# Performance work log

Hardware: AMD Instinct MI355X
Metric: run time of the kernel (lower is better)

The kernel has to match this reference:

```python
import jax, jax.numpy as jnp
import numpy as np

C = 256
B, H, W = 4, 64, 64


def _conv1x1(x, w, b):
    # 1x1 Conv2d == per-pixel channel matmul: w is [C_out, C_in]
    return jnp.einsum('oc,bchw->bohw', w, x) + b[None, :, None, None]


def setup_inputs() -> dict:
    key = jax.random.key(0)
    ks = jax.random.split(key, 9)
    s = 1.0 / np.sqrt(C)  # conv init scale
    return {
        'x': jax.random.normal(ks[0], (B, C, H, W), dtype=jnp.float32),
        'wq': jax.random.normal(ks[1], (C, C), dtype=jnp.float32) * s,
        'bq': jax.random.normal(ks[2], (C,), dtype=jnp.float32) * s,
        'wk': jax.random.normal(ks[3], (C, C), dtype=jnp.float32) * s,
        'bk': jax.random.normal(ks[4], (C,), dtype=jnp.float32) * s,
        'wv': jax.random.normal(ks[5], (C, C), dtype=jnp.float32) * s,
        'bv': jax.random.normal(ks[6], (C,), dtype=jnp.float32) * s,
        'wp': jax.random.normal(ks[7], (C, C), dtype=jnp.float32) * s,
        'bp': jax.random.normal(ks[8], (C,), dtype=jnp.float32) * s,
    }


def reference(x, wq, bq, wk, bk, wv, bv, wp, bp):
    b, c, h, w = x.shape
    n = h * w
    q = _conv1x1(x, wq, bq).reshape(b, c, n)
    k = _conv1x1(x, wk, bk).reshape(b, c, n)
    v = _conv1x1(x, wv, bv).reshape(b, c, n)
    attn = jnp.einsum('bci,bcj->bij', q, k) * (c ** -0.5)  # [B, N, N]
    # NOTE: original torch code softmaxes over dim=1 (the i axis), not -1
    attn = jax.nn.softmax(attn, axis=1)
    out = jnp.einsum('bij,bcj->bci', attn, v).reshape(b, c, h, w)
    return _conv1x1(out, wp, bp)
```

## Files before the change

### kernel.cpp

```cpp
#include <hip/hip_runtime.h>
#include <stdint.h>


#define DI __device__ __forceinline__
typedef __attribute__((ext_vector_type(4))) float f32x4;
typedef __attribute__((ext_vector_type(8))) short s16x8;
typedef __attribute__((ext_vector_type(4))) short s16x4;
typedef __attribute__((ext_vector_type(4))) unsigned short u16x4;

constexpr int C = 256;
constexpr int N = 4096;

DI unsigned short f2bf(float f) {
  unsigned int u = __float_as_uint(f);
  u += 0x7FFFu + ((u >> 16) & 1u);
  return (unsigned short)(u >> 16);
}
DI float bf2f(unsigned short s) { return __uint_as_float(((unsigned int)s) << 16); }

DI f32x4 mfma16(s16x8 a, s16x8 b, f32x4 c) {
  return __builtin_amdgcn_mfma_f32_16x16x32_bf16(a, b, c, 0, 0, 0);
}

__global__ __launch_bounds__(256) void kw_conv(
    const float* __restrict__ wq, const float* __restrict__ wk,
    const float* __restrict__ wv, const float* __restrict__ wp,
    unsigned short* __restrict__ WQ, unsigned short* __restrict__ WK,
    unsigned short* __restrict__ WV, unsigned short* __restrict__ WPH,
    unsigned short* __restrict__ WPL) {
  int idx = (blockIdx.x * 256 + threadIdx.x) * 4;
  f32x4 q = *(const f32x4*)(wq + idx);
  f32x4 k = *(const f32x4*)(wk + idx);
  f32x4 v = *(const f32x4*)(wv + idx);
  f32x4 p = *(const f32x4*)(wp + idx);
  u16x4 oq, ok, ov, oh, ol;
#pragma unroll
  for (int e = 0; e < 4; ++e) {
    oq[e] = f2bf(q[e] * 0.0625f);
    ok[e] = f2bf(k[e]);
    ov[e] = f2bf(v[e]);
    unsigned short h = f2bf(p[e]);
    oh[e] = h;
    ol[e] = f2bf(p[e] - bf2f(h));
  }
  *(u16x4*)(WQ + idx) = oq;
  *(u16x4*)(WK + idx) = ok;
  *(u16x4*)(WV + idx) = ov;
  *(u16x4*)(WPH + idx) = oh;
  *(u16x4*)(WPL + idx) = ol;
}

__global__ __launch_bounds__(256) void k0_transpose(const float* __restrict__ X,
                                                    unsigned short* __restrict__ XT) {
  __shared__ float tile[64 * 65];
  int t = threadIdx.x;
  int wg = blockIdx.x;
  int b = wg >> 8, rem = wg & 255;
  int c0 = (rem >> 6) * 64, n0 = (rem & 63) * 64;
  const float* xb = X + (size_t)b * C * N;
  int cl = t >> 2, ng = (t & 3) * 16;
#pragma unroll
  for (int k = 0; k < 4; ++k) {
    f32x4 v = *(const f32x4*)(xb + (size_t)(c0 + cl) * N + n0 + ng + k * 4);
#pragma unroll
    for (int e = 0; e < 4; ++e) tile[cl * 65 + ng + k * 4 + e] = v[e];
  }
  __syncthreads();
  int nl = t >> 2, cg = (t & 3) * 16;
  unsigned short* xtb = XT + (size_t)b * N * C;
  s16x8 o0v, o1v;
#pragma unroll
  for (int j = 0; j < 8; ++j) o0v[j] = (short)f2bf(tile[(cg + j) * 65 + nl]);
#pragma unroll
  for (int j = 0; j < 8; ++j) o1v[j] = (short)f2bf(tile[(cg + 8 + j) * 65 + nl]);
  *(s16x8*)(xtb + (size_t)(n0 + nl) * C + c0 + cg) = o0v;
  *(s16x8*)(xtb + (size_t)(n0 + nl) * C + c0 + cg + 8) = o1v;
}

__global__ __launch_bounds__(256) void k1_qkv(
    const unsigned short* __restrict__ XT,
    const unsigned short* __restrict__ WQ, const float* __restrict__ bq,
    const unsigned short* __restrict__ WK, const float* __restrict__ bk,
    const unsigned short* __restrict__ WV, const float* __restrict__ bv,
    unsigned short* __restrict__ QT, unsigned short* __restrict__ KT,
    unsigned short* __restrict__ V) {
  int t = threadIdx.x, lane = t & 63, w = t >> 6, l15 = lane & 15, g = lane >> 4;
  int wg = blockIdx.x, b = wg >> 6, nb = wg & 63;
  int n0 = nb * 64;
  const unsigned short* xtb = XT + (size_t)b * N * C;
  const unsigned short* Ws[3] = {WQ, WK, WV};
  const float* Bs[3] = {bq, bk, bv};
#pragma unroll
  for (int np = 0; np < 2; ++np) {
    s16x8 xf[2][8];
#pragma unroll
    for (int n2 = 0; n2 < 2; ++n2)
#pragma unroll
      for (int cc = 0; cc < 8; ++cc)
        xf[n2][cc] = *(const s16x8*)(xtb + (size_t)(n0 + np * 32 + n2 * 16 + l15) * C + cc * 32 + g * 8);
#pragma unroll
    for (int ty = 0; ty < 3; ++ty) {
      float bsc = (ty == 0) ? 0.0625f : 1.0f;
#pragma unroll
      for (int ot = 0; ot < 4; ++ot) {
        int o0 = w * 64 + ot * 16;
        f32x4 bias = *(const f32x4*)(Bs[ty] + o0 + g * 4);
        s16x8 wf[8];
#pragma unroll
        for (int cc = 0; cc < 8; ++cc)
          wf[cc] = *(const s16x8*)(Ws[ty] + (size_t)(o0 + l15) * C + cc * 32 + g * 8);
#pragma unroll
        for (int n2 = 0; n2 < 2; ++n2) {
          f32x4 D = {0.f, 0.f, 0.f, 0.f};
#pragma unroll
          for (int cc = 0; cc < 8; ++cc) D = mfma16(wf[cc], xf[n2][cc], D);
          int n = n0 + np * 32 + n2 * 16 + l15;
          if (ty < 2) {
            s16x4 pk;
#pragma unroll
            for (int r = 0; r < 4; ++r) pk[r] = (short)f2bf(D[r] + bias[r] * bsc);
            unsigned short* dst = (ty == 0 ? QT : KT) + (size_t)b * N * C + (size_t)n * C + o0 + g * 4;
            *(s16x4*)dst = pk;
          } else {
#pragma unroll
            for (int r = 0; r < 4; ++r)
              V[(size_t)b * C * N + (size_t)(o0 + g * 4 + r) * N + n] = f2bf(D[r] + bias[r]);
          }
        }
      }
    }
  }
}

__global__ __launch_bounds__(256, 2) void k2_stats(
    const unsigned short* __restrict__ QT, const unsigned short* __restrict__ KT,
    float* __restrict__ Lp) {
  int t = threadIdx.x, lane = t & 63, w = t >> 6, l15 = lane & 15, g = lane >> 4;
  int wg = blockIdx.x, jb = wg & 31, isplit = (wg >> 5) & 3, b = wg >> 7;
  const unsigned short* qtb = QT + (size_t)b * N * C;
  const unsigned short* ktb = KT + (size_t)b * N * C;
  s16x8 kf[2][8];
#pragma unroll
  for (int jt = 0; jt < 2; ++jt)
#pragma unroll
    for (int cc = 0; cc < 8; ++cc)
      kf[jt][cc] = *(const s16x8*)(ktb + (size_t)(jb * 128 + w * 32 + jt * 16 + l15) * C + cc * 32 + g * 8);
  float sums[2][4];
#pragma unroll
  for (int jt = 0; jt < 2; ++jt)
#pragma unroll
    for (int r = 0; r < 4; ++r) sums[jt][r] = 0.f;
  for (int it = 0; it < 64; ++it) {
    int i0 = isplit * 1024 + it * 16;
    f32x4 D0 = {0.f, 0.f, 0.f, 0.f}, D1 = {0.f, 0.f, 0.f, 0.f};
#pragma unroll
    for (int cc = 0; cc < 8; ++cc) {
      s16x8 qf = *(const s16x8*)(qtb + (size_t)(i0 + l15) * C + cc * 32 + g * 8);
      D0 = mfma16(kf[0][cc], qf, D0);
      D1 = mfma16(kf[1][cc], qf, D1);
    }
#pragma unroll
    for (int r = 0; r < 4; ++r) {
      sums[0][r] += __expf(D0[r] - 12.f);
      sums[1][r] += __expf(D1[r] - 12.f);
    }
  }
#pragma unroll
  for (int off = 1; off < 16; off <<= 1)
#pragma unroll
    for (int jt = 0; jt < 2; ++jt)
#pragma unroll
      for (int r = 0; r < 4; ++r) sums[jt][r] += __shfl_xor(sums[jt][r], off);
  if (l15 == 0) {
#pragma unroll
    for (int jt = 0; jt < 2; ++jt) {
      f32x4 o = {sums[jt][0], sums[jt][1], sums[jt][2], sums[jt][3]};
      *(f32x4*)&Lp[(size_t)(isplit * 4 + b) * N + jb * 128 + w * 32 + jt * 16 + g * 4] = o;
    }
  }
}

__global__ __launch_bounds__(256) void k2b_scale_v(unsigned short* __restrict__ V,
                                                   const float* __restrict__ Lp) {
  int idx4 = (blockIdx.x * 256 + threadIdx.x) * 4;
  int b = idx4 >> 20, n4 = idx4 & (N - 1);
  u16x4 v = *(u16x4*)(V + (size_t)idx4);
  f32x4 lv = *(const f32x4*)(Lp + (size_t)b * N + n4);
#pragma unroll
  for (int s = 1; s < 4; ++s) {
    f32x4 l2 = *(const f32x4*)(Lp + (size_t)(s * 4 + b) * N + n4);
#pragma unroll
    for (int e = 0; e < 4; ++e) lv[e] += l2[e];
  }
  u16x4 o;
#pragma unroll
  for (int e = 0; e < 4; ++e) o[e] = f2bf(bf2f(v[e]) / lv[e]);
  *(u16x4*)(V + (size_t)idx4) = o;
}

__global__ __launch_bounds__(256, 2) void k3_attn(
    const unsigned short* __restrict__ QT, const unsigned short* __restrict__ KT,
    const unsigned short* __restrict__ V, float* __restrict__ OT) {
  __shared__ short K_lds[2][32 * 264];
  __shared__ short V_lds[2][256 * 40];
  __shared__ short P_lds[64 * 40];
  int t = threadIdx.x, lane = t & 63, w = t >> 6, l15 = lane & 15, g = lane >> 4;
  int wg = blockIdx.x;
  int x = wg & 7, b = x >> 1, ib = (x & 1) * 32 + (wg >> 3);
  int jt = w & 1, ip = w >> 1;
  const unsigned short* qtb = QT + (size_t)b * N * C;
  const unsigned short* ktb = KT + (size_t)b * N * C;
  const unsigned short* vb = V + (size_t)b * C * N;
  float* otb = OT + (size_t)b * N * C;
  int krow = t >> 3, kcol = (t & 7) * 32;

  s16x8 qf[2][8];
#pragma unroll
  for (int tt = 0; tt < 2; ++tt)
#pragma unroll
    for (int cc = 0; cc < 8; ++cc)
      qf[tt][cc] = *(const s16x8*)(qtb + (size_t)(ib * 64 + (ip * 2 + tt) * 16 + l15) * C + cc * 32 + g * 8);

  f32x4 acc[4][4];
#pragma unroll
  for (int ct = 0; ct < 4; ++ct)
#pragma unroll
    for (int it = 0; it < 4; ++it) acc[ct][it] = (f32x4){0.f, 0.f, 0.f, 0.f};

  {
    const unsigned short* kg = ktb + (size_t)krow * C + kcol;
    const unsigned short* vg = vb + (size_t)t * N;
#pragma unroll
    for (int k = 0; k < 4; ++k) {
      f32x4 kv = *(const f32x4*)(kg + k * 8);
      f32x4 vv = *(const f32x4*)(vg + k * 8);
      *(f32x4*)&K_lds[0][krow * 264 + kcol + k * 8] = kv;
      *(f32x4*)&V_lds[0][t * 40 + k * 8] = vv;
    }
  }
  __syncthreads();

  for (int ph = 0; ph < 128; ++ph) {
    int cur = ph & 1;
    f32x4 kreg[4], vreg[4];
    if (ph < 127) {
      int J1 = (ph + 1) * 32;
      const unsigned short* kg = ktb + (size_t)(J1 + krow) * C + kcol;
      const unsigned short* vg = vb + (size_t)t * N + J1;
#pragma unroll
      for (int k = 0; k < 4; ++k) {
        kreg[k] = *(const f32x4*)(kg + k * 8);
        vreg[k] = *(const f32x4*)(vg + k * 8);
      }
    }
    s16x8 kf[8];
#pragma unroll
    for (int cc = 0; cc < 8; ++cc)
      kf[cc] = *(const s16x8*)&K_lds[cur][(jt * 16 + l15) * 264 + cc * 32 + g * 8];
    f32x4 D0 = {0.f, 0.f, 0.f, 0.f}, D1 = {0.f, 0.f, 0.f, 0.f};
#pragma unroll
    for (int cc = 0; cc < 8; ++cc) {
      D0 = mfma16(kf[cc], qf[0][cc], D0);
      D1 = mfma16(kf[cc], qf[1][cc], D1);
    }
    s16x4 p0, p1;
#pragma unroll
    for (int r = 0; r < 4; ++r) {
      p0[r] = (short)f2bf(__expf(D0[r] - 12.f));
      p1[r] = (short)f2bf(__expf(D1[r] - 12.f));
    }
    *(s16x4*)&P_lds[((ip * 2 + 0) * 16 + l15) * 40 + jt * 16 + g * 4] = p0;
    *(s16x4*)&P_lds[((ip * 2 + 1) * 16 + l15) * 40 + jt * 16 + g * 4] = p1;
    __syncthreads();
    s16x8 pf[4];
#pragma unroll
    for (int it = 0; it < 4; ++it)
      pf[it] = *(const s16x8*)&P_lds[(it * 16 + l15) * 40 + g * 8];
#pragma unroll
    for (int ct = 0; ct < 4; ++ct) {
      s16x8 vf = *(const s16x8*)&V_lds[cur][(w * 64 + ct * 16 + l15) * 40 + g * 8];
#pragma unroll
      for (int it = 0; it < 4; ++it) acc[ct][it] = mfma16(vf, pf[it], acc[ct][it]);
    }
    if (ph < 127) {
      int nxt = cur ^ 1;
#pragma unroll
      for (int k = 0; k < 4; ++k) {
        *(f32x4*)&K_lds[nxt][krow * 264 + kcol + k * 8] = kreg[k];
        *(f32x4*)&V_lds[nxt][t * 40 + k * 8] = vreg[k];
      }
    }
    __syncthreads();
  }
#pragma unroll
  for (int ct = 0; ct < 4; ++ct)
#pragma unroll
    for (int it = 0; it < 4; ++it)
      *(f32x4*)&otb[(size_t)(ib * 64 + it * 16 + l15) * C + w * 64 + ct * 16 + g * 4] = acc[ct][it];
}

__global__ __launch_bounds__(256) void k4_proj(const float* __restrict__ OT,
                                               const unsigned short* __restrict__ WPH,
                                               const unsigned short* __restrict__ WPL,
                                               const float* __restrict__ bp,
                                               float* __restrict__ OUT) {
  int t = threadIdx.x, lane = t & 63, w = t >> 6, l15 = lane & 15, g = lane >> 4;
  int wg = blockIdx.x, b = wg >> 6, nb = wg & 63;
  const float* otb = OT + (size_t)b * N * C;
  float* ob = OUT + (size_t)b * (size_t)C * N;
  for (int nt = 0; nt < 4; ++nt) {
    s16x8 xh[8], xl[8];
#pragma unroll
    for (int cc = 0; cc < 8; ++cc) {
      const float* p = otb + (size_t)(nb * 64 + nt * 16 + l15) * C + cc * 32 + g * 8;
      f32x4 a = *(const f32x4*)p;
      f32x4 b2 = *(const f32x4*)(p + 4);
      s16x8 h, lo;
#pragma unroll
      for (int e = 0; e < 4; ++e) {
        unsigned short hh = f2bf(a[e]); h[e] = (short)hh; lo[e] = (short)f2bf(a[e] - bf2f(hh));
        unsigned short h2 = f2bf(b2[e]); h[e + 4] = (short)h2; lo[e + 4] = (short)f2bf(b2[e] - bf2f(h2));
      }
      xh[cc] = h; xl[cc] = lo;
    }
#pragma unroll
    for (int ot = 0; ot < 4; ++ot) {
      int o0 = w * 64 + ot * 16;
      f32x4 bias = *(const f32x4*)(bp + o0 + g * 4);
      f32x4 D = {0.f, 0.f, 0.f, 0.f};
#pragma unroll
      for (int cc = 0; cc < 8; ++cc) {
        s16x8 h = *(const s16x8*)(WPH + (size_t)(o0 + l15) * C + cc * 32 + g * 8);
        s16x8 lo = *(const s16x8*)(WPL + (size_t)(o0 + l15) * C + cc * 32 + g * 8);
        D = mfma16(h, xh[cc], D);
        D = mfma16(h, xl[cc], D);
        D = mfma16(lo, xh[cc], D);
      }
#pragma unroll
      for (int r = 0; r < 4; ++r)
        ob[(size_t)(o0 + g * 4 + r) * N + nb * 64 + nt * 16 + l15] = D[r] + bias[r];
    }
  }
}

extern "C" void kernel_launch(void* const* d_in, const int* in_sizes, int n_in,
                              void* d_out, int out_size, void* d_ws, size_t ws_size,
                              hipStream_t stream) {
  const float* x = (const float*)d_in[0];
  const float* wq = (const float*)d_in[1];
  const float* bq = (const float*)d_in[2];
  const float* wk = (const float*)d_in[3];
  const float* bk = (const float*)d_in[4];
  const float* wv = (const float*)d_in[5];
  const float* bv = (const float*)d_in[6];
  const float* wp = (const float*)d_in[7];
  const float* bp = (const float*)d_in[8];
  float* out = (float*)d_out;
  char* ws = (char*)d_ws;
  unsigned short* QT = (unsigned short*)(ws + 0);
  unsigned short* KT = (unsigned short*)(ws + 8388608);
  unsigned short* V  = (unsigned short*)(ws + 16777216);
  unsigned short* WQ = (unsigned short*)(ws + 25165824);
  unsigned short* WK = (unsigned short*)(ws + 25296896);
  unsigned short* WV = (unsigned short*)(ws + 25427968);
  unsigned short* WPH = (unsigned short*)(ws + 25559040);
  unsigned short* WPL = (unsigned short*)(ws + 25690112);
  float* Lp = (float*)(ws + 25821184);
  unsigned short* XT = (unsigned short*)(ws + 26214400);
  float* OT = (float*)(ws + 26214400);

  hipLaunchKernelGGL(kw_conv, dim3(64), dim3(256), 0, stream, wq, wk, wv, wp, WQ, WK, WV, WPH, WPL);
  hipLaunchKernelGGL(k0_transpose, dim3(1024), dim3(256), 0, stream, x, XT);
  hipLaunchKernelGGL(k1_qkv, dim3(256), dim3(256), 0, stream, XT, WQ, bq, WK, bk, WV, bv, QT, KT, V);
  hipLaunchKernelGGL(k2_stats, dim3(512), dim3(256), 0, stream, QT, KT, Lp);
  hipLaunchKernelGGL(k2b_scale_v, dim3(4096), dim3(256), 0, stream, V, Lp);
  hipLaunchKernelGGL(k3_attn, dim3(256), dim3(256), 0, stream, QT, KT, V, OT);
  hipLaunchKernelGGL(k4_proj, dim3(256), dim3(256), 0, stream, OT, WPH, WPL, bp, out);
}
```

Measured before the change: 438.8 us.

## Warp-specialize attention kernel into QK and PV waves using 32x32 MFMA

```diff
diff --git a/kernel.cpp b/kernel.cpp
--- a/kernel.cpp
+++ b/kernel.cpp
@@ -4,6 +4,7 @@
 
 #define DI __device__ __forceinline__
 typedef __attribute__((ext_vector_type(4))) float f32x4;
+typedef __attribute__((ext_vector_type(16))) float f32x16;
 typedef __attribute__((ext_vector_type(8))) short s16x8;
 typedef __attribute__((ext_vector_type(4))) short s16x4;
 typedef __attribute__((ext_vector_type(4))) unsigned short u16x4;
@@ -20,6 +21,15 @@
 
 DI f32x4 mfma16(s16x8 a, s16x8 b, f32x4 c) {
   return __builtin_amdgcn_mfma_f32_16x16x32_bf16(a, b, c, 0, 0, 0);
+}
+DI f32x16 mfma32(s16x8 a, s16x8 b, f32x16 c) {
+  return __builtin_amdgcn_mfma_f32_32x32x16_bf16(a, b, c, 0, 0, 0);
+}
+DI f32x16 zero16() {
+  f32x16 z;
+#pragma unroll
+  for (int e = 0; e < 16; ++e) z[e] = 0.f;
+  return z;
 }
 
 __global__ __launch_bounds__(256) void kw_conv(
@@ -180,123 +190,150 @@
   }
 }
 
-__global__ __launch_bounds__(256) void k2b_scale_v(unsigned short* __restrict__ V,
-                                                   const float* __restrict__ Lp) {
-  int idx4 = (blockIdx.x * 256 + threadIdx.x) * 4;
-  int b = idx4 >> 20, n4 = idx4 & (N - 1);
-  u16x4 v = *(u16x4*)(V + (size_t)idx4);
-  f32x4 lv = *(const f32x4*)(Lp + (size_t)b * N + n4);
-#pragma unroll
-  for (int s = 1; s < 4; ++s) {
-    f32x4 l2 = *(const f32x4*)(Lp + (size_t)(s * 4 + b) * N + n4);
-#pragma unroll
-    for (int e = 0; e < 4; ++e) lv[e] += l2[e];
-  }
-  u16x4 o;
-#pragma unroll
-  for (int e = 0; e < 4; ++e) o[e] = f2bf(bf2f(v[e]) / lv[e]);
-  *(u16x4*)(V + (size_t)idx4) = o;
-}
-
-__global__ __launch_bounds__(256, 2) void k3_attn(
+__global__ __launch_bounds__(256) void k2c_recip(const float* __restrict__ Lp,
+                                                 float* __restrict__ R) {
+  int idx = (blockIdx.x * 256 + threadIdx.x) * 4;
+  int b = idx >> 12, n = idx & (N - 1);
+  f32x4 s = *(const f32x4*)(Lp + (size_t)b * N + n);
+#pragma unroll
+  for (int sl = 1; sl < 4; ++sl) {
+    f32x4 l2 = *(const f32x4*)(Lp + (size_t)(sl * 4 + b) * N + n);
+#pragma unroll
+    for (int e = 0; e < 4; ++e) s[e] += l2[e];
+  }
+  f32x4 o;
+#pragma unroll
+  for (int e = 0; e < 4; ++e) o[e] = 1.0f / s[e];
+  *(f32x4*)(R + idx) = o;
+}
+
+__global__ __launch_bounds__(512, 2) void k3_attn(
     const unsigned short* __restrict__ QT, const unsigned short* __restrict__ KT,
-    const unsigned short* __restrict__ V, float* __restrict__ OT) {
-  __shared__ short K_lds[2][32 * 264];
-  __shared__ short V_lds[2][256 * 40];
-  __shared__ short P_lds[64 * 40];
-  int t = threadIdx.x, lane = t & 63, w = t >> 6, l15 = lane & 15, g = lane >> 4;
+    const unsigned short* __restrict__ V, const float* __restrict__ R,
+    float* __restrict__ OT) {
+  __shared__ short K_lds[64 * 264];
+  __shared__ short V_lds[256 * 72];
+  __shared__ short P_lds[2][64 * 72];
+  int t = threadIdx.x, lane = t & 63, w = t >> 6;
+  int l31 = lane & 31, h = lane >> 5;
   int wg = blockIdx.x;
   int x = wg & 7, b = x >> 1, ib = (x & 1) * 32 + (wg >> 3);
-  int jt = w & 1, ip = w >> 1;
+  int i0 = ib * 64;
   const unsigned short* qtb = QT + (size_t)b * N * C;
   const unsigned short* ktb = KT + (size_t)b * N * C;
   const unsigned short* vb = V + (size_t)b * C * N;
+  const float* rb = R + (size_t)b * N;
   float* otb = OT + (size_t)b * N * C;
-  int krow = t >> 3, kcol = (t & 7) * 32;
-
-  s16x8 qf[2][8];
-#pragma unroll
-  for (int tt = 0; tt < 2; ++tt)
-#pragma unroll
-    for (int cc = 0; cc < 8; ++cc)
-      qf[tt][cc] = *(const s16x8*)(qtb + (size_t)(ib * 64 + (ip * 2 + tt) * 16 + l15) * C + cc * 32 + g * 8);
-
-  f32x4 acc[4][4];
-#pragma unroll
-  for (int ct = 0; ct < 4; ++ct)
-#pragma unroll
-    for (int it = 0; it < 4; ++it) acc[ct][it] = (f32x4){0.f, 0.f, 0.f, 0.f};
-
-  {
-    const unsigned short* kg = ktb + (size_t)krow * C + kcol;
-    const unsigned short* vg = vb + (size_t)t * N;
-#pragma unroll
-    for (int k = 0; k < 4; ++k) {
-      f32x4 kv = *(const f32x4*)(kg + k * 8);
-      f32x4 vv = *(const f32x4*)(vg + k * 8);
-      *(f32x4*)&K_lds[0][krow * 264 + kcol + k * 8] = kv;
-      *(f32x4*)&V_lds[0][t * 40 + k * 8] = vv;
-    }
+  bool isQK = (w < 4);
+  int jt = w & 1, it = (w >> 1) & 1;
+  int pw = w & 3, ct0 = pw * 2;
+  int u = t & 255;
+
+  s16x8 qf[16];
+  f32x16 acc00, acc01, acc10, acc11;
+  if (isQK) {
+#pragma unroll
+    for (int kk = 0; kk < 16; ++kk)
+      qf[kk] = *(const s16x8*)(qtb + (size_t)(i0 + it * 32 + l31) * C + kk * 16 + h * 8);
+#pragma unroll
+    for (int k = 0; k < 8; ++k) {
+      int kr = (u >> 5) + 8 * k;
+      f32x4 kv = *(const f32x4*)(ktb + (size_t)kr * C + (u & 31) * 8);
+      *(f32x4*)&K_lds[kr * 264 + (u & 31) * 8] = kv;
+    }
+  } else {
+    acc00 = zero16(); acc01 = zero16(); acc10 = zero16(); acc11 = zero16();
   }
   __syncthreads();
 
-  for (int ph = 0; ph < 128; ++ph) {
-    int cur = ph & 1;
-    f32x4 kreg[4], vreg[4];
-    if (ph < 127) {
-      int J1 = (ph + 1) * 32;
-      const unsigned short* kg = ktb + (size_t)(J1 + krow) * C + kcol;
-      const unsigned short* vg = vb + (size_t)t * N + J1;
-#pragma unroll
-      for (int k = 0; k < 4; ++k) {
-        kreg[k] = *(const f32x4*)(kg + k * 8);
-        vreg[k] = *(const f32x4*)(vg + k * 8);
-      }
-    }
-    s16x8 kf[8];
-#pragma unroll
-    for (int cc = 0; cc < 8; ++cc)
-      kf[cc] = *(const s16x8*)&K_lds[cur][(jt * 16 + l15) * 264 + cc * 32 + g * 8];
-    f32x4 D0 = {0.f, 0.f, 0.f, 0.f}, D1 = {0.f, 0.f, 0.f, 0.f};
-#pragma unroll
-    for (int cc = 0; cc < 8; ++cc) {
-      D0 = mfma16(kf[cc], qf[0][cc], D0);
-      D1 = mfma16(kf[cc], qf[1][cc], D1);
-    }
-    s16x4 p0, p1;
-#pragma unroll
-    for (int r = 0; r < 4; ++r) {
-      p0[r] = (short)f2bf(__expf(D0[r] - 12.f));
-      p1[r] = (short)f2bf(__expf(D1[r] - 12.f));
-    }
-    *(s16x4*)&P_lds[((ip * 2 + 0) * 16 + l15) * 40 + jt * 16 + g * 4] = p0;
-    *(s16x4*)&P_lds[((ip * 2 + 1) * 16 + l15) * 40 + jt * 16 + g * 4] = p1;
+  for (int p = 0; p <= 64; ++p) {
+    int J0 = p << 6;
+    f32x4 kreg[8], vreg[8];
+    if (isQK) {
+      if (p < 63) {
+        int J1 = J0 + 64;
+#pragma unroll
+        for (int k = 0; k < 8; ++k)
+          kreg[k] = *(const f32x4*)(ktb + (size_t)(J1 + (u >> 5) + 8 * k) * C + (u & 31) * 8);
+      }
+    } else {
+      if (p < 64) {
+#pragma unroll
+        for (int k = 0; k < 8; ++k)
+          vreg[k] = *(const f32x4*)(vb + (size_t)((u >> 3) + 32 * k) * N + J0 + (u & 7) * 8);
+      }
+    }
+    if (isQK) {
+      if (p < 64) {
+        f32x16 Da = zero16(), Db = zero16();
+        const short* kbase = &K_lds[(jt * 32 + l31) * 264 + h * 8];
+#pragma unroll
+        for (int kk = 0; kk < 16; kk += 2) {
+          s16x8 ka = *(const s16x8*)(kbase + kk * 16);
+          s16x8 kb2 = *(const s16x8*)(kbase + kk * 16 + 16);
+          Da = mfma32(ka, qf[kk], Da);
+          Db = mfma32(kb2, qf[kk + 1], Db);
+        }
+        const float* rp = rb + J0 + jt * 32 + h * 4;
+        short* pb = &P_lds[p & 1][(it * 32 + l31) * 72 + jt * 32 + h * 4];
+#pragma unroll
+        for (int q = 0; q < 4; ++q) {
+          f32x4 r4 = *(const f32x4*)(rp + q * 8);
+          s16x4 pk;
+#pragma unroll
+          for (int e = 0; e < 4; ++e)
+            pk[e] = (short)f2bf(__expf(Da[q * 4 + e] + Db[q * 4 + e] - 12.f) * r4[e]);
+          *(s16x4*)(pb + q * 8) = pk;
+        }
+      }
+    } else {
+      if (p >= 1) {
+        const short* pbase = &P_lds[(p - 1) & 1][l31 * 72 + h * 8];
+        const short* vbase = &V_lds[(ct0 * 32 + l31) * 72 + h * 8];
+#pragma unroll
+        for (int kk = 0; kk < 4; ++kk) {
+          s16x8 vf0 = *(const s16x8*)(vbase + kk * 16);
+          s16x8 vf1 = *(const s16x8*)(vbase + 32 * 72 + kk * 16);
+          s16x8 pf0 = *(const s16x8*)(pbase + kk * 16);
+          s16x8 pf1 = *(const s16x8*)(pbase + 32 * 72 + kk * 16);
+          acc00 = mfma32(vf0, pf0, acc00);
+          acc01 = mfma32(vf0, pf1, acc01);
+          acc10 = mfma32(vf1, pf0, acc10);
+          acc11 = mfma32(vf1, pf1, acc11);
+        }
+      }
+    }
     __syncthreads();
-    s16x8 pf[4];
-#pragma unroll
-    for (int it = 0; it < 4; ++it)
-      pf[it] = *(const s16x8*)&P_lds[(it * 16 + l15) * 40 + g * 8];
-#pragma unroll
-    for (int ct = 0; ct < 4; ++ct) {
-      s16x8 vf = *(const s16x8*)&V_lds[cur][(w * 64 + ct * 16 + l15) * 40 + g * 8];
-#pragma unroll
-      for (int it = 0; it < 4; ++it) acc[ct][it] = mfma16(vf, pf[it], acc[ct][it]);
-    }
-    if (ph < 127) {
-      int nxt = cur ^ 1;
-#pragma unroll
-      for (int k = 0; k < 4; ++k) {
-        *(f32x4*)&K_lds[nxt][krow * 264 + kcol + k * 8] = kreg[k];
-        *(f32x4*)&V_lds[nxt][t * 40 + k * 8] = vreg[k];
+    if (isQK) {
+      if (p < 63) {
+#pragma unroll
+        for (int k = 0; k < 8; ++k)
+          *(f32x4*)&K_lds[((u >> 5) + 8 * k) * 264 + (u & 31) * 8] = kreg[k];
+      }
+    } else {
+      if (p < 64) {
+#pragma unroll
+        for (int k = 0; k < 8; ++k)
+          *(f32x4*)&V_lds[((u >> 3) + 32 * k) * 72 + (u & 7) * 8] = vreg[k];
       }
     }
     __syncthreads();
   }
-#pragma unroll
-  for (int ct = 0; ct < 4; ++ct)
-#pragma unroll
-    for (int it = 0; it < 4; ++it)
-      *(f32x4*)&otb[(size_t)(ib * 64 + it * 16 + l15) * C + w * 64 + ct * 16 + g * 4] = acc[ct][it];
+
+  if (!isQK) {
+#pragma unroll
+    for (int q = 0; q < 4; ++q) {
+      f32x4 o;
+      o[0] = acc00[q * 4 + 0]; o[1] = acc00[q * 4 + 1]; o[2] = acc00[q * 4 + 2]; o[3] = acc00[q * 4 + 3];
+      *(f32x4*)&otb[(size_t)(i0 + l31) * C + ct0 * 32 + q * 8 + h * 4] = o;
+      o[0] = acc01[q * 4 + 0]; o[1] = acc01[q * 4 + 1]; o[2] = acc01[q * 4 + 2]; o[3] = acc01[q * 4 + 3];
+      *(f32x4*)&otb[(size_t)(i0 + 32 + l31) * C + ct0 * 32 + q * 8 + h * 4] = o;
+      o[0] = acc10[q * 4 + 0]; o[1] = acc10[q * 4 + 1]; o[2] = acc10[q * 4 + 2]; o[3] = acc10[q * 4 + 3];
+      *(f32x4*)&otb[(size_t)(i0 + l31) * C + (ct0 + 1) * 32 + q * 8 + h * 4] = o;
+      o[0] = acc11[q * 4 + 0]; o[1] = acc11[q * 4 + 1]; o[2] = acc11[q * 4 + 2]; o[3] = acc11[q * 4 + 3];
+      *(f32x4*)&otb[(size_t)(i0 + 32 + l31) * C + (ct0 + 1) * 32 + q * 8 + h * 4] = o;
+    }
+  }
 }
 
 __global__ __launch_bounds__(256) void k4_proj(const float* __restrict__ OT,
@@ -366,6 +403,7 @@
   unsigned short* WPH = (unsigned short*)(ws + 25559040);
   unsigned short* WPL = (unsigned short*)(ws + 25690112);
   float* Lp = (float*)(ws + 25821184);
+  float* R  = (float*)(ws + 26083328);
   unsigned short* XT = (unsigned short*)(ws + 26214400);
   float* OT = (float*)(ws + 26214400);
 
@@ -373,7 +411,7 @@
   hipLaunchKernelGGL(k0_transpose, dim3(1024), dim3(256), 0, stream, x, XT);
   hipLaunchKernelGGL(k1_qkv, dim3(256), dim3(256), 0, stream, XT, WQ, bq, WK, bk, WV, bv, QT, KT, V);
   hipLaunchKernelGGL(k2_stats, dim3(512), dim3(256), 0, stream, QT, KT, Lp);
-  hipLaunchKernelGGL(k2b_scale_v, dim3(4096), dim3(256), 0, stream, V, Lp);
-  hipLaunchKernelGGL(k3_attn, dim3(256), dim3(256), 0, stream, QT, KT, V, OT);
+  hipLaunchKernelGGL(k2c_recip, dim3(16), dim3(256), 0, stream, Lp, R);
+  hipLaunchKernelGGL(k3_attn, dim3(256), dim3(512), 0, stream, QT, KT, V, R, OT);
   hipLaunchKernelGGL(k4_proj, dim3(256), dim3(256), 0, stream, OT, WPH, WPL, bp, out);
 }
```

Measured after the change: 372.8 us. 1.18x faster.
